# Kernel tuning notes

Measured on AMD Instinct MI355X. Metric: run time of the kernel, lower is better.

Reference implementation:

```python
import jax, jax.numpy as jnp
import numpy as np

No_, Nk_, Ni_, D_, F_ = 256, 32, 512, 3, 64

def _quat_scale_to_covar(quats, scales):
    # gsplat convention: quat = (w, x, y, z), normalized; covar = R diag(s^2) R^T
    q = quats / jnp.linalg.norm(quats, axis=-1, keepdims=True)
    w, x, y, z = q[..., 0], q[..., 1], q[..., 2], q[..., 3]
    R = jnp.stack([
        1 - 2 * (y * y + z * z), 2 * (x * y - w * z), 2 * (x * z + w * y),
        2 * (x * y + w * z), 1 - 2 * (x * x + z * z), 2 * (y * z - w * x),
        2 * (x * z - w * y), 2 * (y * z + w * x), 1 - 2 * (x * x + y * y),
    ], axis=-1).reshape(q.shape[:-1] + (3, 3))
    M = R * scales[..., None, :]
    return M @ jnp.swapaxes(M, -1, -2)

def setup_inputs():
    key = jax.random.key(0)
    ks = jax.random.split(key, 8)
    weights = jax.random.uniform(ks[0], (Ni_,)) + 0.1          # positive mixture weights
    means = jax.random.normal(ks[1], (Ni_, D_))
    A = jax.random.normal(ks[2], (Ni_, D_, D_)) * 0.3
    covars = A @ jnp.swapaxes(A, -1, -2) + 0.1 * jnp.eye(D_)   # SPD input covariances
    features = jax.random.normal(ks[3], (Ni_, F_))
    k_weights = jax.random.uniform(ks[4], (No_, Nk_)) + 0.1
    k_means = jax.random.normal(ks[5], (No_, Nk_, D_))
    k_scales = jax.random.uniform(ks[6], (No_, Nk_, D_)) * 0.5 + 0.1
    k_quats = jax.random.normal(ks[7], (No_, Nk_, 4))
    return dict(weights=weights, means=means, covars=covars, features=features,
                k_weights=k_weights, k_means=k_means, k_scales=k_scales, k_quats=k_quats)

def reference(weights, means, covars, features, k_weights, k_means, k_scales, k_quats):
    No, Nk, D = k_means.shape
    # _sample: deterministic 'most important points' = means of top-No weighted components
    _, idx = jax.lax.top_k(weights, No)
    anchor = means[idx]                                   # (No, D)
    comp_means = anchor[:, None, :] + k_means             # (No, Nk, D)
    comp_covars = _quat_scale_to_covar(k_quats, k_scales) # (No, Nk, D, D)
    # GM convolution: outer-product broadcast over input components
    conv_w = k_weights[:, :, None] * weights[None, None, :]               # (No, Nk, Ni)
    conv_m = comp_means[:, :, None, :] + means[None, None, :, :]          # (No, Nk, Ni, D)
    conv_c = comp_covars[:, :, None, :, :] + covars[None, None, :, :, :]  # (No, Nk, Ni, D, D)
    # Moment-matching merge over the Ni axis (dim=2)
    W = conv_w.sum(-1)                                                    # (No, Nk)
    mu = jnp.einsum('oki,okid->okd', conv_w, conv_m) / W[..., None]       # (No, Nk, D)
    diff = conv_m - mu[:, :, None, :]
    second = conv_c + diff[..., :, None] * diff[..., None, :]
    cov = jnp.einsum('oki,okide->okde', conv_w, second) / W[..., None, None]  # (No, Nk, D, D)
    return W, mu, cov
```

## Files before the change

### kernel.cpp

```cpp
#include <hip/hip_runtime.h>

namespace {

constexpr int NO  = 256;
constexpr int NK  = 32;
constexpr int NI  = 512;
constexpr int BLK = 1024;
constexpr int NB  = (NO * NK) / BLK;

using u32 = unsigned int;
using u64 = unsigned long long;

__global__ __launch_bounds__(BLK) void gm_fused_kernel(
    const float* __restrict__ weights,
    const float* __restrict__ means,
    const float* __restrict__ covars,
    const float* __restrict__ k_weights,
    const float* __restrict__ k_means,
    const float* __restrict__ k_scales,
    const float* __restrict__ k_quats,
    float* __restrict__ out)
{
  __shared__ __align__(16) u64 keys[NI];
  __shared__ int   rhi[NI];
  __shared__ float anchors[NO * 3];
  __shared__ float red[16][6];
  __shared__ float stats[10];

  const int tid   = threadIdx.x;
  const int lane  = tid & 63;
  const int wave  = tid >> 6;
  const bool lower = tid < NI;
  const int item  = lower ? tid : tid - NI;

  const int t = blockIdx.x * BLK + tid;
  const int o = t >> 5;
  const float  kw  = k_weights[t];
  const float  km0 = k_means[3 * t + 0];
  const float  km1 = k_means[3 * t + 1];
  const float  km2 = k_means[3 * t + 2];
  const float4 q4  = *(const float4*)(k_quats + 4 * t);
  const float  s0  = k_scales[3 * t + 0];
  const float  s1  = k_scales[3 * t + 1];
  const float  s2  = k_scales[3 * t + 2];

  const float w  = weights[item];
  const float m0 = means[3 * item + 0];
  const float m1 = means[3 * item + 1];
  const float m2 = means[3 * item + 2];

  float acc[6] = {0.f, 0.f, 0.f, 0.f, 0.f, 0.f};
  if (lower) {
    acc[0] = w;
    acc[1] = w * m0; acc[2] = w * m1; acc[3] = w * m2;
    keys[item] = ((u64)__float_as_uint(w) << 32) | (u32)(NI - 1 - item);
  } else {
    const float c00 = covars[9 * item + 0];
    const float c01 = covars[9 * item + 1];
    const float c02 = covars[9 * item + 2];
    const float c11 = covars[9 * item + 4];
    const float c12 = covars[9 * item + 5];
    const float c22 = covars[9 * item + 8];
    acc[0] = w * (c00 + m0 * m0);
    acc[1] = w * (c01 + m0 * m1);
    acc[2] = w * (c02 + m0 * m2);
    acc[3] = w * (c11 + m1 * m1);
    acc[4] = w * (c12 + m1 * m2);
    acc[5] = w * (c22 + m2 * m2);
  }

  #pragma unroll
  for (int off = 32; off > 0; off >>= 1) {
    #pragma unroll
    for (int e = 0; e < 6; ++e) acc[e] += __shfl_down(acc[e], off, 64);
  }
  if (lane == 0) {
    #pragma unroll
    for (int e = 0; e < 6; ++e) red[wave][e] = acc[e];
  }
  __syncthreads();

  if (tid < 10) {
    float s = 0.f;
    if (tid < 4) {
      #pragma unroll
      for (int wv = 0; wv < 8; ++wv) s += red[wv][tid];
    } else {
      #pragma unroll
      for (int wv = 8; wv < 16; ++wv) s += red[wv][tid - 4];
    }
    stats[tid] = s;
  }

  const u64 mykey = keys[item];
  const ulonglong2* seg = (const ulonglong2*)(keys + (lower ? 0 : NI / 2));
  int r0 = 0, r1 = 0, r2 = 0, r3 = 0;
  #pragma unroll 8
  for (int p = 0; p < (NI / 2) / 4; ++p) {
    const ulonglong2 ka = seg[2 * p + 0];
    const ulonglong2 kb = seg[2 * p + 1];
    r0 += (int)(ka.x > mykey);
    r1 += (int)(ka.y > mykey);
    r2 += (int)(kb.x > mykey);
    r3 += (int)(kb.y > mykey);
  }
  const int r = (r0 + r1) + (r2 + r3);
  if (!lower) rhi[item] = r;
  __syncthreads();

  if (lower) {
    const int rank = r + rhi[item];
    if (rank < NO) {
      anchors[3 * rank + 0] = m0;
      anchors[3 * rank + 1] = m1;
      anchors[3 * rank + 2] = m2;
    }
  }
  __syncthreads();

  const float S   = stats[0];
  const float inv = 1.f / S;
  const float b0 = stats[1] * inv, b1 = stats[2] * inv, b2 = stats[3] * inv;
  const float C00 = stats[4] * inv - b0 * b0;
  const float C01 = stats[5] * inv - b0 * b1;
  const float C02 = stats[6] * inv - b0 * b2;
  const float C11 = stats[7] * inv - b1 * b1;
  const float C12 = stats[8] * inv - b1 * b2;
  const float C22 = stats[9] * inv - b2 * b2;
  const float a0 = anchors[3 * o + 0];
  const float a1 = anchors[3 * o + 1];
  const float a2 = anchors[3 * o + 2];

  float qw = q4.x, qx = q4.y, qy = q4.z, qz = q4.w;
  const float rn = rsqrtf(qw * qw + qx * qx + qy * qy + qz * qz);
  qw *= rn; qx *= rn; qy *= rn; qz *= rn;

  float R[3][3];
  R[0][0] = 1.f - 2.f * (qy * qy + qz * qz);
  R[0][1] = 2.f * (qx * qy - qw * qz);
  R[0][2] = 2.f * (qx * qz + qw * qy);
  R[1][0] = 2.f * (qx * qy + qw * qz);
  R[1][1] = 1.f - 2.f * (qx * qx + qz * qz);
  R[1][2] = 2.f * (qy * qz - qw * qx);
  R[2][0] = 2.f * (qx * qz - qw * qy);
  R[2][1] = 2.f * (qy * qz + qw * qx);
  R[2][2] = 1.f - 2.f * (qx * qx + qy * qy);

  const float sc[3] = { s0, s1, s2 };
  float M[3][3];
  #pragma unroll
  for (int rr = 0; rr < 3; ++rr)
    #pragma unroll
    for (int cc = 0; cc < 3; ++cc)
      M[rr][cc] = R[rr][cc] * sc[cc];

  const float Cb[9] = { C00, C01, C02, C01, C11, C12, C02, C12, C22 };
  float cov[9];
  #pragma unroll
  for (int rr = 0; rr < 3; ++rr) {
    #pragma unroll
    for (int cc = 0; cc < 3; ++cc) {
      float a = Cb[3 * rr + cc];
      #pragma unroll
      for (int e = 0; e < 3; ++e) a += M[rr][e] * M[cc][e];
      cov[3 * rr + cc] = a;
    }
  }

  out[t] = kw * S;
  const int mu_base = NO * NK + 3 * t;
  out[mu_base + 0] = a0 + km0 + b0;
  out[mu_base + 1] = a1 + km1 + b1;
  out[mu_base + 2] = a2 + km2 + b2;
  const int cov_base = NO * NK * 4 + 9 * t;
  #pragma unroll
  for (int e = 0; e < 9; ++e)
    out[cov_base + e] = cov[e];
}

}

extern "C" void kernel_launch(void* const* d_in, const int* in_sizes, int n_in,
                              void* d_out, int out_size, void* d_ws, size_t ws_size,
                              hipStream_t stream) {
  const float* weights   = (const float*)d_in[0];
  const float* means     = (const float*)d_in[1];
  const float* covars    = (const float*)d_in[2];
  const float* k_weights = (const float*)d_in[4];
  const float* k_means   = (const float*)d_in[5];
  const float* k_scales  = (const float*)d_in[6];
  const float* k_quats   = (const float*)d_in[7];

  gm_fused_kernel<<<NB, BLK, 0, stream>>>(weights, means, covars,
                                          k_weights, k_means, k_scales, k_quats,
                                          (float*)d_out);
}
```

Measured before the change: 14.31 us.

## Split rank computation across thread pairs and hoist quaternion covariance before barrier

The rank loop now has two threads per key, each scanning half the key array, with the halves combined by a lane shuffle. This removes one __syncthreads and the shared rhi array. Each block keeps only the anchors for its own 32-output window, and the quaternion-to-covariance math moves before the first barrier so it can overlap the reduction wait. Means are staged in shared memory for the anchor writes, which adds a little LDS traffic.

```diff
diff --git a/kernel.cpp b/kernel.cpp
--- a/kernel.cpp
+++ b/kernel.cpp
@@ -7,6 +7,7 @@
 constexpr int NI  = 512;
 constexpr int BLK = 1024;
 constexpr int NB  = (NO * NK) / BLK;
+constexpr int OWIN = BLK / NK;
 
 using u32 = unsigned int;
 using u64 = unsigned long long;
@@ -22,8 +23,8 @@
     float* __restrict__ out)
 {
   __shared__ __align__(16) u64 keys[NI];
-  __shared__ int   rhi[NI];
-  __shared__ float anchors[NO * 3];
+  __shared__ float sm[NI * 3];
+  __shared__ float anchors[OWIN * 3];
   __shared__ float red[16][6];
   __shared__ float stats[10];
 
@@ -32,9 +33,9 @@
   const int wave  = tid >> 6;
   const bool lower = tid < NI;
   const int item  = lower ? tid : tid - NI;
-
-  const int t = blockIdx.x * BLK + tid;
-  const int o = t >> 5;
+  const int b     = blockIdx.x;
+
+  const int t = b * BLK + tid;
   const float  kw  = k_weights[t];
   const float  km0 = k_means[3 * t + 0];
   const float  km1 = k_means[3 * t + 1];
@@ -54,6 +55,7 @@
     acc[0] = w;
     acc[1] = w * m0; acc[2] = w * m1; acc[3] = w * m2;
     keys[item] = ((u64)__float_as_uint(w) << 32) | (u32)(NI - 1 - item);
+    sm[3 * item + 0] = m0; sm[3 * item + 1] = m1; sm[3 * item + 2] = m2;
   } else {
     const float c00 = covars[9 * item + 0];
     const float c01 = covars[9 * item + 1];
@@ -78,6 +80,43 @@
     #pragma unroll
     for (int e = 0; e < 6; ++e) red[wave][e] = acc[e];
   }
+
+  float Q[9];
+  {
+    float qw = q4.x, qx = q4.y, qy = q4.z, qz = q4.w;
+    const float rn = rsqrtf(qw * qw + qx * qx + qy * qy + qz * qz);
+    qw *= rn; qx *= rn; qy *= rn; qz *= rn;
+
+    float R[3][3];
+    R[0][0] = 1.f - 2.f * (qy * qy + qz * qz);
+    R[0][1] = 2.f * (qx * qy - qw * qz);
+    R[0][2] = 2.f * (qx * qz + qw * qy);
+    R[1][0] = 2.f * (qx * qy + qw * qz);
+    R[1][1] = 1.f - 2.f * (qx * qx + qz * qz);
+    R[1][2] = 2.f * (qy * qz - qw * qx);
+    R[2][0] = 2.f * (qx * qz - qw * qy);
+    R[2][1] = 2.f * (qy * qz + qw * qx);
+    R[2][2] = 1.f - 2.f * (qx * qx + qy * qy);
+
+    const float sc[3] = { s0, s1, s2 };
+    float M[3][3];
+    #pragma unroll
+    for (int rr = 0; rr < 3; ++rr)
+      #pragma unroll
+      for (int cc = 0; cc < 3; ++cc)
+        M[rr][cc] = R[rr][cc] * sc[cc];
+
+    #pragma unroll
+    for (int rr = 0; rr < 3; ++rr)
+      #pragma unroll
+      for (int cc = 0; cc < 3; ++cc) {
+        float a = 0.f;
+        #pragma unroll
+        for (int e = 0; e < 3; ++e) a += M[rr][e] * M[cc][e];
+        Q[3 * rr + cc] = a;
+      }
+  }
+
   __syncthreads();
 
   if (tid < 10) {
@@ -92,28 +131,34 @@
     stats[tid] = s;
   }
 
-  const u64 mykey = keys[item];
-  const ulonglong2* seg = (const ulonglong2*)(keys + (lower ? 0 : NI / 2));
-  int r0 = 0, r1 = 0, r2 = 0, r3 = 0;
-  #pragma unroll 8
-  for (int p = 0; p < (NI / 2) / 4; ++p) {
-    const ulonglong2 ka = seg[2 * p + 0];
-    const ulonglong2 kb = seg[2 * p + 1];
+  const int  pair  = tid >> 1;
+  const u64  mykey = keys[pair];
+  const ulonglong2* seg = (const ulonglong2*)(keys + (tid & 1) * (NI / 2));
+  int r0 = 0, r1 = 0, r2 = 0, r3 = 0, r4 = 0, r5 = 0, r6 = 0, r7 = 0;
+  #pragma unroll 4
+  for (int p = 0; p < 32; ++p) {
+    const ulonglong2 ka = seg[4 * p + 0];
+    const ulonglong2 kb = seg[4 * p + 1];
+    const ulonglong2 kc = seg[4 * p + 2];
+    const ulonglong2 kd = seg[4 * p + 3];
     r0 += (int)(ka.x > mykey);
     r1 += (int)(ka.y > mykey);
     r2 += (int)(kb.x > mykey);
     r3 += (int)(kb.y > mykey);
-  }
-  const int r = (r0 + r1) + (r2 + r3);
-  if (!lower) rhi[item] = r;
-  __syncthreads();
-
-  if (lower) {
-    const int rank = r + rhi[item];
-    if (rank < NO) {
-      anchors[3 * rank + 0] = m0;
-      anchors[3 * rank + 1] = m1;
-      anchors[3 * rank + 2] = m2;
+    r4 += (int)(kc.x > mykey);
+    r5 += (int)(kc.y > mykey);
+    r6 += (int)(kd.x > mykey);
+    r7 += (int)(kd.y > mykey);
+  }
+  int r = ((r0 + r1) + (r2 + r3)) + ((r4 + r5) + (r6 + r7));
+  const int rank = r + __shfl_xor(r, 1, 64);
+
+  if ((tid & 1) == 0) {
+    const int lr = rank - OWIN * b;
+    if ((unsigned)lr < (unsigned)OWIN) {
+      anchors[3 * lr + 0] = sm[3 * pair + 0];
+      anchors[3 * lr + 1] = sm[3 * pair + 1];
+      anchors[3 * lr + 2] = sm[3 * pair + 2];
     }
   }
   __syncthreads();
@@ -127,55 +172,23 @@
   const float C11 = stats[7] * inv - b1 * b1;
   const float C12 = stats[8] * inv - b1 * b2;
   const float C22 = stats[9] * inv - b2 * b2;
-  const float a0 = anchors[3 * o + 0];
-  const float a1 = anchors[3 * o + 1];
-  const float a2 = anchors[3 * o + 2];
-
-  float qw = q4.x, qx = q4.y, qy = q4.z, qz = q4.w;
-  const float rn = rsqrtf(qw * qw + qx * qx + qy * qy + qz * qz);
-  qw *= rn; qx *= rn; qy *= rn; qz *= rn;
-
-  float R[3][3];
-  R[0][0] = 1.f - 2.f * (qy * qy + qz * qz);
-  R[0][1] = 2.f * (qx * qy - qw * qz);
-  R[0][2] = 2.f * (qx * qz + qw * qy);
-  R[1][0] = 2.f * (qx * qy + qw * qz);
-  R[1][1] = 1.f - 2.f * (qx * qx + qz * qz);
-  R[1][2] = 2.f * (qy * qz - qw * qx);
-  R[2][0] = 2.f * (qx * qz - qw * qy);
-  R[2][1] = 2.f * (qy * qz + qw * qx);
-  R[2][2] = 1.f - 2.f * (qx * qx + qy * qy);
-
-  const float sc[3] = { s0, s1, s2 };
-  float M[3][3];
-  #pragma unroll
-  for (int rr = 0; rr < 3; ++rr)
-    #pragma unroll
-    for (int cc = 0; cc < 3; ++cc)
-      M[rr][cc] = R[rr][cc] * sc[cc];
-
-  const float Cb[9] = { C00, C01, C02, C01, C11, C12, C02, C12, C22 };
-  float cov[9];
-  #pragma unroll
-  for (int rr = 0; rr < 3; ++rr) {
-    #pragma unroll
-    for (int cc = 0; cc < 3; ++cc) {
-      float a = Cb[3 * rr + cc];
-      #pragma unroll
-      for (int e = 0; e < 3; ++e) a += M[rr][e] * M[cc][e];
-      cov[3 * rr + cc] = a;
-    }
-  }
+
+  const int ol = tid >> 5;
+  const float a0 = anchors[3 * ol + 0];
+  const float a1 = anchors[3 * ol + 1];
+  const float a2 = anchors[3 * ol + 2];
 
   out[t] = kw * S;
   const int mu_base = NO * NK + 3 * t;
   out[mu_base + 0] = a0 + km0 + b0;
   out[mu_base + 1] = a1 + km1 + b1;
   out[mu_base + 2] = a2 + km2 + b2;
+
+  const float Cb[9] = { C00, C01, C02, C01, C11, C12, C02, C12, C22 };
   const int cov_base = NO * NK * 4 + 9 * t;
   #pragma unroll
   for (int e = 0; e < 9; ++e)
-    out[cov_base + e] = cov[e];
+    out[cov_base + e] = Q[e] + Cb[e];
 }
 
 }
```

Result: slower. 16.65 us (+16.4%).
